# Kernel optimization log

Hardware: AMD Instinct MI355X
Metric: run time of the kernel (lower is better)

The kernel has to match this reference:

```python
import jax, jax.numpy as jnp
import numpy as np

B, N, IN_DIM = 16, 768, 16
HID, EMB, N_LAYERS, N_HEADS = 64, 128, 2, 8


def setup_inputs() -> dict:
    key = jax.random.key(0)
    ks = jax.random.split(key, 10)
    s = lambda fan_in: 1.0 / np.sqrt(fan_in)
    inp = {
        "x": jax.random.normal(ks[0], (B, N, IN_DIM), dtype=jnp.float32),
        "ip_w": jax.random.uniform(ks[1], (IN_DIM, HID), jnp.float32, -s(IN_DIM), s(IN_DIM)),
        "ip_b": jax.random.uniform(ks[2], (HID,), jnp.float32, -s(IN_DIM), s(IN_DIM)),
        # layer 0: in_features = HID; layer 1: in_features = HID * N_HEADS
        "gat_w0": jax.random.uniform(ks[3], (N_HEADS, HID, HID), jnp.float32, -s(HID), s(HID)),
        "gat_a0": jax.random.uniform(ks[4], (N_HEADS, 2 * HID), jnp.float32, -s(2 * HID), s(2 * HID)),
        "gat_w1": jax.random.uniform(ks[5], (N_HEADS, HID * N_HEADS, HID), jnp.float32, -s(HID * N_HEADS), s(HID * N_HEADS)),
        "gat_a1": jax.random.uniform(ks[6], (N_HEADS, 2 * HID), jnp.float32, -s(2 * HID), s(2 * HID)),
        "proj_w": jax.random.uniform(ks[7], (HID * N_HEADS, EMB), jnp.float32, -s(HID * N_HEADS), s(HID * N_HEADS)),
        "proj_b": jax.random.uniform(ks[8], (EMB,), jnp.float32, -s(HID * N_HEADS), s(HID * N_HEADS)),
    }
    return inp


def _gat_layer(h, W, a):
    # h: [B, N, F_in]; W: [H, F_in, F_out]; a: [H, 2*F_out]
    Wh = jnp.einsum("bnf,hfo->bhno", h, W)  # [B,H,N,F_out]
    f_out = W.shape[-1]
    a1, a2 = a[:, :f_out], a[:, f_out:]
    # additive attention decomposed: e_ij = leakyrelu(a1.Wh_i + a2.Wh_j)
    s1 = jnp.einsum("bhno,ho->bhn", Wh, a1)
    s2 = jnp.einsum("bhno,ho->bhn", Wh, a2)
    e = jax.nn.leaky_relu(s1[..., :, None] + s2[..., None, :], negative_slope=0.2)
    # adj = ones -> mask is a no-op; dense softmax over neighbors
    att = jax.nn.softmax(e, axis=-1)  # [B,H,N,N]
    hp = jnp.einsum("bhnm,bhmo->bhno", att, Wh)
    b, hds, n, f = hp.shape
    return hp.transpose(0, 2, 1, 3).reshape(b, n, hds * f)  # concat heads


def reference(x, ip_w, ip_b, gat_w0, gat_a0, gat_w1, gat_a1, proj_w, proj_b):
    h = x @ ip_w + ip_b  # input_proj
    h = _gat_layer(h, gat_w0, gat_a0)
    h = _gat_layer(h, gat_w1, gat_a1)
    # dropout identity (eval); final activation (ELU) is never applied in forward
    return h @ proj_w + proj_b  # [B, N, EMB]
```

## Files before the change

### kernel.cpp

```cpp
#include <hip/hip_runtime.h>
#include <hip/hip_bf16.h>


#define B_ 16
#define N_ 768
#define IN_DIM_ 16
#define HID_ 64
#define EMB_ 128
#define NH_ 8
#define LOG2E_ 1.4426950408889634f

typedef __attribute__((ext_vector_type(4))) float f32x4;
typedef __attribute__((ext_vector_type(8))) short bf16x8;
typedef __attribute__((ext_vector_type(4))) short bf16x4;

typedef __attribute__((address_space(1))) const unsigned int gu32;
typedef __attribute__((address_space(3))) unsigned int lu32;

static __device__ __forceinline__ void gload_lds16(const void* g, void* l) {
    __builtin_amdgcn_global_load_lds((gu32*)g, (lu32*)l, 16, 0, 0);
}

static __device__ __forceinline__ short f2bf(float x) {
    __hip_bfloat16 b = __float2bfloat16(x);
    return *reinterpret_cast<short*>(&b);
}

__global__ __launch_bounds__(256) void k_prep(const float* __restrict__ x,
                                              const float* __restrict__ ipw,
                                              const float* __restrict__ ipb,
                                              const float* __restrict__ w1,
                                              const float* __restrict__ pw,
                                              const float* __restrict__ w0,
                                              const float* __restrict__ a1g,
                                              const float* __restrict__ a0g,
                                              ushort* __restrict__ h0A,
                                              ushort* __restrict__ W1f,
                                              ushort* __restrict__ pwf,
                                              ushort* __restrict__ W0f,
                                              ushort* __restrict__ u1F,
                                              ushort* __restrict__ u0F) {
    const int bid = blockIdx.x;
    const int tid = threadIdx.x;
    if (bid < 384) {
        const int t = bid * 256 + tid;
        const int lane = t & 63;
        const int kt = (t >> 6) & 1;
        const int rtg = t >> 7;
        const int row = rtg * 16 + (lane & 15);
        const int k0 = kt * 32 + (lane >> 4) * 8;
        const float* xr = x + row * IN_DIM_;
        float xv[IN_DIM_];
#pragma unroll
        for (int f = 0; f < IN_DIM_; ++f) xv[f] = xr[f];
        bf16x8 v;
#pragma unroll
        for (int j = 0; j < 8; ++j) {
            float acc = ipb[k0 + j];
#pragma unroll
            for (int f = 0; f < IN_DIM_; ++f) acc = fmaf(xv[f], ipw[f * HID_ + k0 + j], acc);
            v[j] = f2bf(acc);
        }
        *(bf16x8*)&h0A[t * 8] = v;
        return;
    }
    if (bid < 560) {
        int t = (bid - 384) * 256 + tid;
        if (t < 32768) {
            int lane = t & 63, nt = (t >> 6) & 3, kt = (t >> 8) & 15, h = t >> 12;
            int k0 = kt * 32 + (lane >> 4) * 8;
            int col = nt * 16 + (lane & 15);
            const float* src = w1 + (h * 512 + k0) * 64 + col;
            bf16x8 v;
#pragma unroll
            for (int j = 0; j < 8; ++j) v[j] = f2bf(src[j * 64]);
            *(bf16x8*)&W1f[t * 8] = v;
        } else if (t < 40960) {
            int u = t - 32768;
            int lane = u & 63, nt = (u >> 6) & 7, kt = u >> 9;
            int k0 = kt * 32 + (lane >> 4) * 8;
            int col = nt * 16 + (lane & 15);
            const float* src = pw + k0 * 128 + col;
            bf16x8 v;
#pragma unroll
            for (int j = 0; j < 8; ++j) v[j] = f2bf(src[j * 128]);
            *(bf16x8*)&pwf[u * 8] = v;
        } else {
            int u = t - 40960;
            int lane = u & 63, nt = (u >> 6) & 3, kt = (u >> 8) & 1, h = u >> 9;
            int k0 = kt * 32 + (lane >> 4) * 8;
            int col = nt * 16 + (lane & 15);
            const float* src = w0 + (h * 64 + k0) * 64 + col;
            bf16x8 v;
#pragma unroll
            for (int j = 0; j < 8; ++j) v[j] = f2bf(src[j * 64]);
            *(bf16x8*)&W0f[u * 8] = v;
        }
        return;
    }
    int ub = bid - 560;
    const float* W;
    const float* A;
    ushort* dst;
    if (ub < 128) {
        int h = ub >> 4, kt = ub & 15;
        W = w1 + (h * 512 + kt * 32) * 64;
        A = a1g + h * 128;
        dst = u1F + (h * 16 + kt) * 512;
    } else {
        int v2 = ub - 128;
        int h = v2 >> 1, kt = v2 & 1;
        W = w0 + (h * 64 + kt * 32) * 64;
        A = a0g + h * 128;
        dst = u0F + (h * 2 + kt) * 512;
    }
    ((unsigned int*)dst)[tid] = 0u;
    __syncthreads();
    const int sel = tid >> 7, kl = (tid >> 2) & 31, og4 = tid & 3;
    const float* Wr = W + kl * 64 + og4 * 16;
    const float* Ar = A + sel * 64 + og4 * 16;
    float r = 0.f;
#pragma unroll
    for (int q = 0; q < 4; ++q) {
        float4 wv = *(const float4*)&Wr[q * 4];
        float4 av = *(const float4*)&Ar[q * 4];
        r += wv.x * av.x + wv.y * av.y + wv.z * av.z + wv.w * av.w;
    }
    r += __shfl_xor(r, 1);
    r += __shfl_xor(r, 2);
    if (og4 == 0)
        dst[((kl >> 3) * 16 + sel) * 8 + (kl & 7)] = (ushort)f2bf(r * LOG2E_);
}

template <int KT>
__global__ __launch_bounds__(768, 3) void k_gat(const ushort* __restrict__ Afrag,
                                                const ushort* __restrict__ Bfrag,
                                                const ushort* __restrict__ uF,
                                                ushort* __restrict__ hpA) {
    __shared__ __align__(16) char smem[98304];
    __shared__ __align__(16) float s1s[N_];
    __shared__ __align__(16) float s2s[N_];
    __shared__ __align__(16) float e2s[N_];
    __shared__ __align__(16) float f2s[N_];
    ushort* whf = (ushort*)smem;

    const int bid = blockIdx.x;
    const int b = bid & 15;
    const int hh = bid >> 4;
    const int h = hh >> 1;
    const int half = hh & 1;

    const int tid = threadIdx.x;
    const int lane = tid & 63;
    const int w = tid >> 6;
    const int lg = lane >> 4;
    const int ll = lane & 15;

    if constexpr (KT == 16) {
        const ushort* src = Bfrag + h * 16 * 2048;
        for (int c = w; c < 64; c += 12)
            gload_lds16(src + c * 512 + lane * 8, (char*)smem + c * 1024);
        __syncthreads();
    }

    f32x4 acc[4][4];
    f32x4 accs[4];
#pragma unroll
    for (int i = 0; i < 4; ++i) {
        accs[i] = (f32x4){0.f, 0.f, 0.f, 0.f};
#pragma unroll
        for (int nt = 0; nt < 4; ++nt) acc[i][nt] = (f32x4){0.f, 0.f, 0.f, 0.f};
    }

    const int rt_base = b * 48 + w * 4;
    auto loadA4 = [&](bf16x8* dst, int kt) {
#pragma unroll
        for (int i = 0; i < 4; ++i)
            dst[i] = *(const bf16x8*)&Afrag[((rt_base + i) * KT + kt) * 512 + lane * 8];
    };
    auto loadB4 = [&](bf16x8* dst, int kt) {
        if constexpr (KT == 16) {
#pragma unroll
            for (int nt = 0; nt < 4; ++nt)
                dst[nt] = *(const bf16x8*)&whf[kt * 2048 + nt * 512 + lane * 8];
        } else {
#pragma unroll
            for (int nt = 0; nt < 4; ++nt)
                dst[nt] = *(const bf16x8*)&Bfrag[((h * 2 + kt) * 4 + nt) * 512 + lane * 8];
        }
    };
    auto stepA = [&](const bf16x8* afr, const bf16x8* bfr, bf16x8 ufr) {
#pragma unroll
        for (int i = 0; i < 4; ++i) {
#pragma unroll
            for (int nt = 0; nt < 4; ++nt)
                acc[i][nt] = __builtin_amdgcn_mfma_f32_16x16x32_bf16(afr[i], bfr[nt], acc[i][nt], 0, 0, 0);
            accs[i] = __builtin_amdgcn_mfma_f32_16x16x32_bf16(afr[i], ufr, accs[i], 0, 0, 0);
        }
    };

    {
        bf16x8 aA[4], aB[4];
        loadA4(aA, 0);
        for (int kt = 0; kt < KT; kt += 2) {
            loadA4(aB, kt + 1);
            bf16x8 bfr[4];
            loadB4(bfr, kt);
            bf16x8 ufr = *(const bf16x8*)&uF[(h * KT + kt) * 512 + lane * 8];
            stepA(aA, bfr, ufr);
            if (kt + 2 < KT) loadA4(aA, kt + 2);
            loadB4(bfr, kt + 1);
            ufr = *(const bf16x8*)&uF[(h * KT + kt + 1) * 512 + lane * 8];
            stepA(aB, bfr, ufr);
        }
    }
    if constexpr (KT == 16) __syncthreads();

#pragma unroll
    for (int i = 0; i < 4; ++i) {
        const int rt = w * 4 + i;
        const int lp = ((rt * 2 + (lg >> 1)) & 3) * 16 + ll;
        const int j0 = 4 * (lg & 1);
#pragma unroll
        for (int nt = 0; nt < 4; ++nt) {
            bf16x4 pk;
#pragma unroll
            for (int reg = 0; reg < 4; ++reg) pk[reg] = f2bf(acc[i][nt][reg]);
            *(bf16x4*)&whf[(((rt >> 1) * 4 + nt) * 64 + lp) * 8 + j0] = pk;
        }
#pragma unroll
        for (int reg = 0; reg < 4; ++reg) {
            const int row = rt * 16 + lg * 4 + reg;
            if (ll == 0) s1s[row] = accs[i][reg];
            else if (ll == 1) s2s[row] = accs[i][reg];
        }
    }
    __syncthreads();

    for (int i = tid; i < N_; i += 768) {
        float t2 = s2s[i];
        e2s[i] = exp2f(t2);
        f2s[i] = exp2f(0.2f * t2);
    }
    const int qbase = half * 384 + w * 32;
    float e1v[2], f1v[2];
#pragma unroll
    for (int mt = 0; mt < 2; ++mt) {
        float t1 = s1s[qbase + mt * 16 + ll];
        e1v[mt] = exp2f(t1);
        f1v[mt] = exp2f(0.2f * t1);
    }
    __syncthreads();

    f32x4 pacc[2][4];
    f32x4 dacc[2];
#pragma unroll
    for (int mt = 0; mt < 2; ++mt) {
        dacc[mt] = (f32x4){0.f, 0.f, 0.f, 0.f};
#pragma unroll
        for (int nt = 0; nt < 4; ++nt) pacc[mt][nt] = (f32x4){0.f, 0.f, 0.f, 0.f};
    }
    bf16x8 onesB;
#pragma unroll
    for (int j = 0; j < 8; ++j) onesB[j] = (ll == 0) ? (short)0x3F80 : (short)0;

    auto loadP = [&](bf16x8* bq, float* ee, float* ff, int kt) {
#pragma unroll
        for (int nt = 0; nt < 4; ++nt)
            bq[nt] = *(const bf16x8*)&whf[kt * 2048 + nt * 512 + lane * 8];
        float4 t0 = *(const float4*)&e2s[kt * 32 + lg * 8];
        float4 t1 = *(const float4*)&e2s[kt * 32 + lg * 8 + 4];
        float4 t2 = *(const float4*)&f2s[kt * 32 + lg * 8];
        float4 t3 = *(const float4*)&f2s[kt * 32 + lg * 8 + 4];
        ee[0] = t0.x; ee[1] = t0.y; ee[2] = t0.z; ee[3] = t0.w;
        ee[4] = t1.x; ee[5] = t1.y; ee[6] = t1.z; ee[7] = t1.w;
        ff[0] = t2.x; ff[1] = t2.y; ff[2] = t2.z; ff[3] = t2.w;
        ff[4] = t3.x; ff[5] = t3.y; ff[6] = t3.z; ff[7] = t3.w;
    };
    auto stepB = [&](const bf16x8* bq, const float* ee, const float* ff) {
#pragma unroll
        for (int mt = 0; mt < 2; ++mt) {
            bf16x8 af;
#pragma unroll
            for (int j = 0; j < 8; ++j)
                af[j] = f2bf(fmaxf(e1v[mt] * ee[j], f1v[mt] * ff[j]));
            dacc[mt] = __builtin_amdgcn_mfma_f32_16x16x32_bf16(af, onesB, dacc[mt], 0, 0, 0);
#pragma unroll
            for (int nt = 0; nt < 4; ++nt)
                pacc[mt][nt] = __builtin_amdgcn_mfma_f32_16x16x32_bf16(af, bq[nt], pacc[mt][nt], 0, 0, 0);
        }
    };

    {
        bf16x8 bqA[4], bqB[4];
        float eA[8], fA[8], eB[8], fB[8];
        loadP(bqA, eA, fA, 0);
        for (int kt = 0; kt < 24; kt += 2) {
            loadP(bqB, eB, fB, kt + 1);
            stepB(bqA, eA, fA);
            if (kt + 2 < 24) loadP(bqA, eA, fA, kt + 2);
            stepB(bqB, eB, fB);
        }
    }
    __syncthreads();

    char* hb8 = smem;
#pragma unroll
    for (int mt = 0; mt < 2; ++mt) {
#pragma unroll
        for (int reg = 0; reg < 4; ++reg) {
            const int rl = w * 32 + mt * 16 + lg * 4 + reg;
            const float dv = __shfl(dacc[mt][reg], lane & 0x30);
            const float inv = 1.0f / dv;
            const int swz = (rl & 7) << 4;
#pragma unroll
            for (int nt = 0; nt < 4; ++nt) {
                int c = nt * 16 + ll;
                *(ushort*)(hb8 + rl * 128 + ((c * 2) ^ swz)) =
                    (ushort)f2bf(pacc[mt][nt][reg] * inv);
            }
        }
    }
    __syncthreads();

#pragma unroll
    for (int rt2 = 0; rt2 < 2; ++rt2) {
#pragma unroll
        for (int kc = 0; kc < 2; ++kc) {
            const int rtl = w * 2 + rt2;
            const int row = rtl * 16 + ll;
            bf16x8 v = *(const bf16x8*)(hb8 + row * 128 +
                                        ((kc * 64 + lg * 16) ^ ((row & 7) << 4)));
            const int rtg = b * 48 + half * 24 + rtl;
            *(bf16x8*)&hpA[((rtg * 16) + (h * 2 + kc)) * 512 + lane * 8] = v;
        }
    }
}

__global__ __launch_bounds__(256) void k_projm(const ushort* __restrict__ hpA,
                                               const ushort* __restrict__ pwf,
                                               const float* __restrict__ bias,
                                               float* __restrict__ out) {
    const int blk = blockIdx.x;
    const int lane = threadIdx.x & 63;
    const int w = threadIdx.x >> 6;
    const int wrow = w >> 1, wcol = w & 1;
    const int lg = lane >> 4;
    const int ll = lane & 15;

    f32x4 acc[4];
#pragma unroll
    for (int nt = 0; nt < 4; ++nt) acc[nt] = (f32x4){0.f, 0.f, 0.f, 0.f};

    const int rt = blk * 2 + wrow;
    for (int kt = 0; kt < 16; ++kt) {
        bf16x8 afr = *(const bf16x8*)&hpA[((rt * 16) + kt) * 512 + lane * 8];
        bf16x8 bfr[4];
#pragma unroll
        for (int nt = 0; nt < 4; ++nt)
            bfr[nt] = *(const bf16x8*)&pwf[((kt * 8) + wcol * 4 + nt) * 512 + lane * 8];
#pragma unroll
        for (int nt = 0; nt < 4; ++nt)
            acc[nt] = __builtin_amdgcn_mfma_f32_16x16x32_bf16(afr, bfr[nt], acc[nt], 0, 0, 0);
    }

#pragma unroll
    for (int reg = 0; reg < 4; ++reg) {
        const int row = blk * 32 + wrow * 16 + lg * 4 + reg;
#pragma unroll
        for (int nt = 0; nt < 4; ++nt) {
            const int col = wcol * 64 + nt * 16 + ll;
            out[row * EMB_ + col] = acc[nt][reg] + bias[col];
        }
    }
}

extern "C" void kernel_launch(void* const* d_in, const int* in_sizes, int n_in,
                              void* d_out, int out_size, void* d_ws, size_t ws_size,
                              hipStream_t stream) {
    const float* x    = (const float*)d_in[0];
    const float* ip_w = (const float*)d_in[1];
    const float* ip_b = (const float*)d_in[2];
    const float* gw0  = (const float*)d_in[3];
    const float* ga0  = (const float*)d_in[4];
    const float* gw1  = (const float*)d_in[5];
    const float* ga1  = (const float*)d_in[6];
    const float* pw   = (const float*)d_in[7];
    const float* pb   = (const float*)d_in[8];
    float* out = (float*)d_out;

    ushort* h0A  = (ushort*)d_ws;
    ushort* hpA0 = h0A + 786432;
    ushort* hpA1 = hpA0 + 6291456;
    ushort* W1f  = hpA1 + 6291456;
    ushort* pwf  = W1f + 262144;
    ushort* W0f  = pwf + 65536;
    ushort* u1F  = W0f + 32768;
    ushort* u0F  = u1F + 65536;

    k_prep<<<704, 256, 0, stream>>>(x, ip_w, ip_b, gw1, pw, gw0, ga1, ga0,
                                    h0A, W1f, pwf, W0f, u1F, u0F);
    k_gat<2><<<256, 768, 0, stream>>>(h0A, W0f, u0F, hpA0);
    k_gat<16><<<256, 768, 0, stream>>>(hpA0, W1f, u1F, hpA1);
    k_projm<<<(B_ * N_) / 32, 256, 0, stream>>>(hpA1, pwf, pb, out);
}
```

Baseline: 145.7 us.

## Replace dense GAT softmax aggregation with sorted prefix-sum evaluation

Since leaky-relu of s1+s2 splits on the sign of s1+s2, the attention aggregation is rewritten as a sort of s2 followed by prefix sums of exp-weighted Wh values. Each query row then needs only a binary search and a lookup of two prefix sums, replacing the O(N^2) MFMA attention. Activations move from MFMA fragment layout to row-major, and outputs are scattered per query. The change adds in-block bitonic sorts with many barriers, serial per-column loops and strided 2-byte global stores, which may cost more than the attention work they replace.

```diff
diff --git a/kernel.cpp b/kernel.cpp
--- a/kernel.cpp
+++ b/kernel.cpp
@@ -13,6 +13,7 @@
 typedef __attribute__((ext_vector_type(4))) float f32x4;
 typedef __attribute__((ext_vector_type(8))) short bf16x8;
 typedef __attribute__((ext_vector_type(4))) short bf16x4;
+typedef unsigned long long u64;
 
 typedef __attribute__((address_space(1))) const unsigned int gu32;
 typedef __attribute__((address_space(3))) unsigned int lu32;
@@ -20,10 +21,35 @@
 static __device__ __forceinline__ void gload_lds16(const void* g, void* l) {
     __builtin_amdgcn_global_load_lds((gu32*)g, (lu32*)l, 16, 0, 0);
 }
-
 static __device__ __forceinline__ short f2bf(float x) {
     __hip_bfloat16 b = __float2bfloat16(x);
     return *reinterpret_cast<short*>(&b);
+}
+static __device__ __forceinline__ float bf2f(ushort u) {
+    unsigned int v = ((unsigned int)u) << 16;
+    union { unsigned int i; float f; } c; c.i = v; return c.f;
+}
+static __device__ __forceinline__ unsigned int fenc(float f) {
+    union { float f; unsigned int i; } c; c.f = f;
+    unsigned int u = c.i;
+    return (u & 0x80000000u) ? ~u : (u | 0x80000000u);
+}
+
+static __device__ void bitonic(u64* a, int SZ, int tid, int nthr) {
+    for (int k = 2; k <= SZ; k <<= 1) {
+        for (int j = k >> 1; j > 0; j >>= 1) {
+            __syncthreads();
+            for (int t = tid; t < (SZ >> 1); t += nthr) {
+                int i = ((t & ~(j - 1)) << 1) | (t & (j - 1));
+                int l = i | j;
+                bool up = ((i & k) == 0);
+                u64 x = a[i], y = a[l];
+                bool sw = up ? (x > y) : (x < y);
+                if (sw) { a[i] = y; a[l] = x; }
+            }
+        }
+    }
+    __syncthreads();
 }
 
 __global__ __launch_bounds__(256) void k_prep(const float* __restrict__ x,
@@ -34,7 +60,7 @@
                                               const float* __restrict__ w0,
                                               const float* __restrict__ a1g,
                                               const float* __restrict__ a0g,
-                                              ushort* __restrict__ h0A,
+                                              ushort* __restrict__ h0r,
                                               ushort* __restrict__ W1f,
                                               ushort* __restrict__ pwf,
                                               ushort* __restrict__ W0f,
@@ -44,11 +70,8 @@
     const int tid = threadIdx.x;
     if (bid < 384) {
         const int t = bid * 256 + tid;
-        const int lane = t & 63;
-        const int kt = (t >> 6) & 1;
-        const int rtg = t >> 7;
-        const int row = rtg * 16 + (lane & 15);
-        const int k0 = kt * 32 + (lane >> 4) * 8;
+        const int row = t >> 3;
+        const int o0 = (t & 7) * 8;
         const float* xr = x + row * IN_DIM_;
         float xv[IN_DIM_];
 #pragma unroll
@@ -56,12 +79,12 @@
         bf16x8 v;
 #pragma unroll
         for (int j = 0; j < 8; ++j) {
-            float acc = ipb[k0 + j];
-#pragma unroll
-            for (int f = 0; f < IN_DIM_; ++f) acc = fmaf(xv[f], ipw[f * HID_ + k0 + j], acc);
+            float acc = ipb[o0 + j];
+#pragma unroll
+            for (int f = 0; f < IN_DIM_; ++f) acc = fmaf(xv[f], ipw[f * HID_ + o0 + j], acc);
             v[j] = f2bf(acc);
         }
-        *(bf16x8*)&h0A[t * 8] = v;
+        *(bf16x8*)&h0r[(size_t)row * 64 + o0] = v;
         return;
     }
     if (bid < 560) {
@@ -133,16 +156,19 @@
 }
 
 template <int KT>
-__global__ __launch_bounds__(768, 3) void k_gat(const ushort* __restrict__ Afrag,
+__global__ __launch_bounds__(768, 3) void k_gat(const ushort* __restrict__ Arow,
                                                 const ushort* __restrict__ Bfrag,
                                                 const ushort* __restrict__ uF,
-                                                ushort* __restrict__ hpA) {
-    __shared__ __align__(16) char smem[98304];
-    __shared__ __align__(16) float s1s[N_];
-    __shared__ __align__(16) float s2s[N_];
-    __shared__ __align__(16) float e2s[N_];
-    __shared__ __align__(16) float f2s[N_];
-    ushort* whf = (ushort*)smem;
+                                                ushort* __restrict__ hpO) {
+    constexpr int KW = KT * 32;
+    __shared__ __align__(16) ushort whf[49152];
+    __shared__ __align__(16) float s1s[N_], s2s[N_];
+    __shared__ __align__(16) u64 sbuf[1024];
+    __shared__ __align__(16) float ts[N_], es[N_], fs[N_], ep[N_], fp[N_];
+    __shared__ __align__(16) float e1a[384], f1a[384], ivd[384];
+    __shared__ __align__(16) float CE[12 * 64], CF[12 * 64];
+    __shared__ __align__(16) float wte[12], wtf[12];
+    __shared__ __align__(16) ushort prm[N_];
 
     const int bid = blockIdx.x;
     const int b = bid & 15;
@@ -159,7 +185,7 @@
     if constexpr (KT == 16) {
         const ushort* src = Bfrag + h * 16 * 2048;
         for (int c = w; c < 64; c += 12)
-            gload_lds16(src + c * 512 + lane * 8, (char*)smem + c * 1024);
+            gload_lds16(src + c * 512 + lane * 8, (char*)whf + c * 1024);
         __syncthreads();
     }
 
@@ -172,11 +198,11 @@
         for (int nt = 0; nt < 4; ++nt) acc[i][nt] = (f32x4){0.f, 0.f, 0.f, 0.f};
     }
 
-    const int rt_base = b * 48 + w * 4;
+    const ushort* Ab = Arow + (size_t)(b * 768) * KW;
     auto loadA4 = [&](bf16x8* dst, int kt) {
 #pragma unroll
         for (int i = 0; i < 4; ++i)
-            dst[i] = *(const bf16x8*)&Afrag[((rt_base + i) * KT + kt) * 512 + lane * 8];
+            dst[i] = *(const bf16x8*)&Ab[(size_t)(w * 64 + i * 16 + ll) * KW + kt * 32 + lg * 8];
     };
     auto loadB4 = [&](bf16x8* dst, int kt) {
         if constexpr (KT == 16) {
@@ -237,107 +263,124 @@
     }
     __syncthreads();
 
-    for (int i = tid; i < N_; i += 768) {
-        float t2 = s2s[i];
-        e2s[i] = exp2f(t2);
-        f2s[i] = exp2f(0.2f * t2);
-    }
-    const int qbase = half * 384 + w * 32;
-    float e1v[2], f1v[2];
-#pragma unroll
-    for (int mt = 0; mt < 2; ++mt) {
-        float t1 = s1s[qbase + mt * 16 + ll];
-        e1v[mt] = exp2f(t1);
-        f1v[mt] = exp2f(0.2f * t1);
-    }
-    __syncthreads();
-
-    f32x4 pacc[2][4];
-    f32x4 dacc[2];
-#pragma unroll
-    for (int mt = 0; mt < 2; ++mt) {
-        dacc[mt] = (f32x4){0.f, 0.f, 0.f, 0.f};
-#pragma unroll
-        for (int nt = 0; nt < 4; ++nt) pacc[mt][nt] = (f32x4){0.f, 0.f, 0.f, 0.f};
-    }
-    bf16x8 onesB;
-#pragma unroll
-    for (int j = 0; j < 8; ++j) onesB[j] = (ll == 0) ? (short)0x3F80 : (short)0;
-
-    auto loadP = [&](bf16x8* bq, float* ee, float* ff, int kt) {
-#pragma unroll
-        for (int nt = 0; nt < 4; ++nt)
-            bq[nt] = *(const bf16x8*)&whf[kt * 2048 + nt * 512 + lane * 8];
-        float4 t0 = *(const float4*)&e2s[kt * 32 + lg * 8];
-        float4 t1 = *(const float4*)&e2s[kt * 32 + lg * 8 + 4];
-        float4 t2 = *(const float4*)&f2s[kt * 32 + lg * 8];
-        float4 t3 = *(const float4*)&f2s[kt * 32 + lg * 8 + 4];
-        ee[0] = t0.x; ee[1] = t0.y; ee[2] = t0.z; ee[3] = t0.w;
-        ee[4] = t1.x; ee[5] = t1.y; ee[6] = t1.z; ee[7] = t1.w;
-        ff[0] = t2.x; ff[1] = t2.y; ff[2] = t2.z; ff[3] = t2.w;
-        ff[4] = t3.x; ff[5] = t3.y; ff[6] = t3.z; ff[7] = t3.w;
+    for (int i = tid; i < 1024; i += 768)
+        sbuf[i] = (i < N_) ? ((((u64)fenc(s2s[i])) << 32) | (u64)i) : ~0ull;
+    bitonic(sbuf, 1024, tid, 768);
+
+    if (tid < N_) {
+        int m = (int)(unsigned int)sbuf[tid];
+        prm[tid] = (ushort)m;
+        float t = s2s[m];
+        ts[tid] = t;
+        es[tid] = exp2f(t);
+        fs[tid] = exp2f(0.2f * t);
+    }
+    __syncthreads();
+
+    {
+        float ve = es[w * 64 + lane];
+        float vf = fs[w * 64 + lane];
+        float ie = ve, jf = vf;
+        for (int off = 1; off < 64; off <<= 1) {
+            float ue = __shfl_up(ie, off);
+            float uf = __shfl_up(jf, off);
+            if (lane >= off) { ie += ue; jf += uf; }
+        }
+        if (lane == 63) { wte[w] = ie; wtf[w] = jf; }
+        float eloc = ie - ve, floc = jf - vf;
+        __syncthreads();
+        float oe = 0.f, of2 = 0.f;
+        for (int ww = 0; ww < w; ++ww) { oe += wte[ww]; of2 += wtf[ww]; }
+        ep[w * 64 + lane] = eloc + oe;
+        fp[w * 64 + lane] = floc + of2;
+    }
+    __syncthreads();
+
+    int myk = 0;
+    if (tid < 384) {
+        const int ng = half * 384 + tid;
+        const float t1 = s1s[ng];
+        const float e1 = exp2f(t1);
+        const float f1 = exp2f(0.2f * t1);
+        const float v = -t1;
+        int lo = 0, hi = N_;
+        while (lo < hi) { int mid = (lo + hi) >> 1; if (ts[mid] < v) lo = mid + 1; else hi = mid; }
+        myk = lo;
+        const float etot = ep[N_ - 1] + es[N_ - 1];
+        const float ftot = fp[N_ - 1] + fs[N_ - 1];
+        const float epk = (myk < N_) ? ep[myk] : etot;
+        const float fpk = (myk < N_) ? fp[myk] : ftot;
+        const float d = e1 * (etot - epk) + f1 * fpk;
+        e1a[tid] = e1; f1a[tid] = f1; ivd[tid] = 1.0f / d;
+    }
+    __syncthreads();
+
+    if (tid < 512)
+        sbuf[tid] = (tid < 384) ? (u64)(((unsigned int)myk << 9) | (unsigned int)tid) : ~0ull;
+    bitonic(sbuf, 512, tid, 768);
+
+    const int c = w;
+    auto whval = [&](int m) {
+        return bf2f(whf[(m >> 5) * 2048 + (lane >> 4) * 512 +
+                        (((m >> 3) & 3) * 16 + (lane & 15)) * 8 + (m & 7)]);
     };
-    auto stepB = [&](const bf16x8* bq, const float* ee, const float* ff) {
-#pragma unroll
-        for (int mt = 0; mt < 2; ++mt) {
-            bf16x8 af;
-#pragma unroll
-            for (int j = 0; j < 8; ++j)
-                af[j] = f2bf(fmaxf(e1v[mt] * ee[j], f1v[mt] * ff[j]));
-            dacc[mt] = __builtin_amdgcn_mfma_f32_16x16x32_bf16(af, onesB, dacc[mt], 0, 0, 0);
-#pragma unroll
-            for (int nt = 0; nt < 4; ++nt)
-                pacc[mt][nt] = __builtin_amdgcn_mfma_f32_16x16x32_bf16(af, bq[nt], pacc[mt][nt], 0, 0, 0);
-        }
+    {
+        float SE = 0.f, SF = 0.f;
+        for (int i = 0; i < 64; ++i) {
+            const int gi = c * 64 + i;
+            const float whv = whval(prm[gi]);
+            SE = fmaf(es[gi], whv, SE);
+            SF = fmaf(fs[gi], whv, SF);
+        }
+        CE[c * 64 + lane] = SE;
+        CF[c * 64 + lane] = SF;
+    }
+    __syncthreads();
+
+    float PE = 0.f, PF = 0.f, Etot = 0.f;
+    for (int cc = 0; cc < 12; ++cc) {
+        const float ve = CE[cc * 64 + lane];
+        Etot += ve;
+        if (cc < c) { PE += ve; PF += CF[cc * 64 + lane]; }
+    }
+
+    auto LB512 = [&](u64 t) {
+        int lo = 0, hi = 512;
+        while (lo < hi) { int mid = (lo + hi) >> 1; if (sbuf[mid] < t) lo = mid + 1; else hi = mid; }
+        return lo;
     };
-
-    {
-        bf16x8 bqA[4], bqB[4];
-        float eA[8], fA[8], eB[8], fB[8];
-        loadP(bqA, eA, fA, 0);
-        for (int kt = 0; kt < 24; kt += 2) {
-            loadP(bqB, eB, fB, kt + 1);
-            stepB(bqA, eA, fA);
-            if (kt + 2 < 24) loadP(bqA, eA, fA, kt + 2);
-            stepB(bqB, eB, fB);
-        }
-    }
-    __syncthreads();
-
-    char* hb8 = smem;
-#pragma unroll
-    for (int mt = 0; mt < 2; ++mt) {
-#pragma unroll
-        for (int reg = 0; reg < 4; ++reg) {
-            const int rl = w * 32 + mt * 16 + lg * 4 + reg;
-            const float dv = __shfl(dacc[mt][reg], lane & 0x30);
-            const float inv = 1.0f / dv;
-            const int swz = (rl & 7) << 4;
-#pragma unroll
-            for (int nt = 0; nt < 4; ++nt) {
-                int c = nt * 16 + ll;
-                *(ushort*)(hb8 + rl * 128 + ((c * 2) ^ swz)) =
-                    (ushort)f2bf(pacc[mt][nt][reg] * inv);
-            }
-        }
-    }
-    __syncthreads();
-
-#pragma unroll
-    for (int rt2 = 0; rt2 < 2; ++rt2) {
-#pragma unroll
-        for (int kc = 0; kc < 2; ++kc) {
-            const int rtl = w * 2 + rt2;
-            const int row = rtl * 16 + ll;
-            bf16x8 v = *(const bf16x8*)(hb8 + row * 128 +
-                                        ((kc * 64 + lg * 16) ^ ((row & 7) << 4)));
-            const int rtg = b * 48 + half * 24 + rtl;
-            *(bf16x8*)&hpA[((rtg * 16) + (h * 2 + kc)) * 512 + lane * 8] = v;
-        }
-    }
-}
-
-__global__ __launch_bounds__(256) void k_projm(const ushort* __restrict__ hpA,
+    const int loB = LB512(((u64)(c * 64)) << 9);
+    const int hiB = (c == 11) ? LB512(((u64)769) << 9) : LB512(((u64)((c + 1) * 64)) << 9);
+
+    const size_t rowG0 = (size_t)(b * 768 + half * 384);
+    ushort* outb = hpO + (size_t)h * 64 + lane;
+    int ptr = loB;
+    float SEl = 0.f, SFl = 0.f;
+    for (int i = 0; i < 64; ++i) {
+        const unsigned int target = (unsigned int)(c * 64 + i);
+        while (ptr < hiB) {
+            const u64 key = sbuf[ptr];
+            if ((unsigned int)(key >> 9) != target) break;
+            const int n = (int)(key & 511u);
+            const float val = (e1a[n] * (Etot - (PE + SEl)) + f1a[n] * (PF + SFl)) * ivd[n];
+            outb[(rowG0 + n) * 512] = (ushort)f2bf(val);
+            ++ptr;
+        }
+        const int gi = c * 64 + i;
+        const float whv = whval(prm[gi]);
+        SEl = fmaf(es[gi], whv, SEl);
+        SFl = fmaf(fs[gi], whv, SFl);
+    }
+    while (ptr < hiB) {
+        const u64 key = sbuf[ptr];
+        const int n = (int)(key & 511u);
+        const float val = (e1a[n] * (Etot - (PE + SEl)) + f1a[n] * (PF + SFl)) * ivd[n];
+        outb[(rowG0 + n) * 512] = (ushort)f2bf(val);
+        ++ptr;
+    }
+}
+
+__global__ __launch_bounds__(256) void k_projm(const ushort* __restrict__ hp1,
                                                const ushort* __restrict__ pwf,
                                                const float* __restrict__ bias,
                                                float* __restrict__ out) {
@@ -354,7 +397,7 @@
 
     const int rt = blk * 2 + wrow;
     for (int kt = 0; kt < 16; ++kt) {
-        bf16x8 afr = *(const bf16x8*)&hpA[((rt * 16) + kt) * 512 + lane * 8];
+        bf16x8 afr = *(const bf16x8*)&hp1[(size_t)(rt * 16 + ll) * 512 + kt * 32 + lg * 8];
         bf16x8 bfr[4];
 #pragma unroll
         for (int nt = 0; nt < 4; ++nt)
@@ -389,18 +432,18 @@
     const float* pb   = (const float*)d_in[8];
     float* out = (float*)d_out;
 
-    ushort* h0A  = (ushort*)d_ws;
-    ushort* hpA0 = h0A + 786432;
-    ushort* hpA1 = hpA0 + 6291456;
-    ushort* W1f  = hpA1 + 6291456;
-    ushort* pwf  = W1f + 262144;
-    ushort* W0f  = pwf + 65536;
-    ushort* u1F  = W0f + 32768;
-    ushort* u0F  = u1F + 65536;
+    ushort* h0r = (ushort*)d_ws;
+    ushort* hp0 = h0r + 786432;
+    ushort* hp1 = hp0 + 6291456;
+    ushort* W1f = hp1 + 6291456;
+    ushort* pwf = W1f + 262144;
+    ushort* W0f = pwf + 65536;
+    ushort* u1F = W0f + 32768;
+    ushort* u0F = u1F + 65536;
 
     k_prep<<<704, 256, 0, stream>>>(x, ip_w, ip_b, gw1, pw, gw0, ga1, ga0,
-                                    h0A, W1f, pwf, W0f, u1F, u0F);
-    k_gat<2><<<256, 768, 0, stream>>>(h0A, W0f, u0F, hpA0);
-    k_gat<16><<<256, 768, 0, stream>>>(hpA0, W1f, u1F, hpA1);
-    k_projm<<<(B_ * N_) / 32, 256, 0, stream>>>(hpA1, pwf, pb, out);
-}
+                                    h0r, W1f, pwf, W0f, u1F, u0F);
+    k_gat<2><<<256, 768, 0, stream>>>(h0r, W0f, u0F, hp0);
+    k_gat<16><<<256, 768, 0, stream>>>(hp0, W1f, u1F, hp1);
+    k_projm<<<(B_ * N_) / 32, 256, 0, stream>>>(hp1, pwf, pb, out);
+}
```

New measurement: 285.0 us. +95.6%, slower.
